# Optimization experiments

Hardware: AMD Instinct MI355X
Metric: run time of the kernel (lower is better)

## Reference

```python
import jax, jax.numpy as jnp
import numpy as np
from jax.scipy.special import digamma

# Dims (see init_kwargs): pose P=4 -> D=16, stem A=128, primary caps B=32,
# classes C=10, class-caps kernel K=6 (== primary feature map size), 3 routing iters.
P, D, A, B, C, K, ITER = 4, 16, 128, 32, 10, 6, 3
N = B * K * K                                    # input capsules routed to each class capsule
ALPHA0, KAPPA0, NU0 = 1.0, 1.0, float(D + 1)     # Dirichlet/Normal-Wishart priors (m0=0, Psi0=I, cov='diag')
BN_EPS, EPS = 1e-5, 1e-8


def conv2d(x, w, s):
    return jax.lax.conv_general_dilated(x, w, (s, s), 'VALID',
                                        dimension_numbers=('NCHW', 'OIHW', 'NCHW'))


def bn(x, gamma, beta, axes):
    # batch-norm with batch statistics (training-mode math)
    mu = x.mean(axes, keepdims=True)
    var = x.var(axes, keepdims=True)
    return (x - mu) * jax.lax.rsqrt(var + BN_EPS) * gamma + beta


def setup_inputs():
    key = jax.random.key(0)
    ks = jax.random.split(key, 4)
    f32 = jnp.float32
    x = jax.random.normal(ks[0], (128, 3, 32, 32), dtype=f32)
    conv1_w = jax.random.normal(ks[1], (A, 3, 5, 5), dtype=f32) * 0.1
    bn1_g = jnp.ones((A,), f32); bn1_b = jnp.zeros((A,), f32)
    prim_w = jax.random.normal(ks[2], (B * D + B, A, 3, 3), dtype=f32) * 0.05
    bna_g = jnp.ones((B,), f32); bna_b = jnp.zeros((B,), f32)
    bnp_g = jnp.ones((B,), f32); bnp_b = jnp.zeros((B,), f32)
    W_ij = jax.random.normal(ks[3], (B, C, K, K, P, P), dtype=f32) * 0.3
    return dict(x=x, conv1_w=conv1_w, bn1_g=bn1_g, bn1_b=bn1_b, prim_w=prim_w,
                bna_g=bna_g, bna_b=bna_b, bnp_g=bnp_g, bnp_b=bnp_b, W_ij=W_ij)


def _vb_stats(Ra, V):
    # Ra: (b,N,C) responsibility * input activation; V: (b,N,C,D) votes
    Nj = Ra.sum(1) + EPS                                         # (b,C)
    xbar = jnp.einsum('bnc,bncd->bcd', Ra, V) / Nj[..., None]    # weighted vote mean
    diff = V - xbar[:, None]
    sigma = jnp.einsum('bnc,bncd->bcd', Ra, diff * diff) / Nj[..., None]  # diag cov
    kappa = KAPPA0 + Nj
    m = Nj[..., None] * xbar / kappa[..., None]                  # posterior mean (m0 = 0)
    nu = NU0 + Nj
    Psi = 1.0 + Nj[..., None] * sigma + (KAPPA0 * Nj / kappa)[..., None] * xbar * xbar  # Psi0 = I (diag)
    return Nj, kappa, m, nu, Psi


def _expectations(Nj, nu, Psi, d_idx):
    alpha = ALPHA0 + Nj
    E_lnpi = digamma(alpha) - digamma(alpha.sum(-1, keepdims=True))
    E_lnLam = (digamma(0.5 * (nu[..., None] + 1.0 - d_idx)).sum(-1)
               + D * jnp.log(2.0) - jnp.log(Psi).sum(-1))
    return E_lnpi, E_lnLam


def reference(x, conv1_w, bn1_g, bn1_b, prim_w, bna_g, bna_b, bnp_g, bnp_b, W_ij):
    b = x.shape[0]
    # --- stem: Conv5x5/s2 + BN + ReLU ---
    h = conv2d(x, conv1_w, 2)                                    # (b,A,14,14)
    h = jax.nn.relu(bn(h, bn1_g[None, :, None, None], bn1_b[None, :, None, None], (0, 2, 3)))
    # --- primary capsules: Conv3x3/s2 -> poses + activations ---
    pc = conv2d(h, prim_w, 2)                                    # (b,B*D+B,6,6)
    poses, a = pc[:, :B * D], pc[:, B * D:]
    a = jax.nn.sigmoid(bn(a, bna_g[None, :, None, None], bna_b[None, :, None, None], (0, 2, 3)))
    poses = bn(poses.reshape(b, B, D, K, K),
               bnp_g[None, :, None, None, None], bnp_b[None, :, None, None, None], (0, 2, 3, 4))
    poses = poses.reshape(b, B, P, P, K, K)
    # --- class capsules: votes V = W_ij @ pose, kernel covers whole 6x6 map ---
    V = jnp.einsum('icxypq,biqrxy->bicxypr', W_ij, poses)        # (b,B,C,K,K,P,P)
    V = V.transpose(0, 1, 3, 4, 2, 5, 6).reshape(b, N, C, D)
    a_i = a.reshape(b, N)
    # --- variational Bayes routing (diag Normal-Wishart, ITER iterations) ---
    d_idx = jnp.arange(1, D + 1, dtype=x.dtype)
    R = jnp.full((b, N, C), 1.0 / C, dtype=x.dtype)
    for t in range(ITER):
        Nj, kappa, m, nu, Psi = _vb_stats(R * a_i[:, :, None], V)
        if t < ITER - 1:
            E_lnpi, E_lnLam = _expectations(Nj, nu, Psi, d_idx)
            dm = V - m[:, None]
            quad = D / kappa[:, None, :] + nu[:, None, :] * jnp.einsum('bncd,bcd->bnc', dm * dm, 1.0 / Psi)
            lnp = (E_lnpi[:, None] + 0.5 * E_lnLam[:, None]
                   - 0.5 * D * jnp.log(2.0 * jnp.pi) - 0.5 * quad)
            R = jax.nn.softmax(lnp, axis=-1)
    E_lnpi, E_lnLam = _expectations(Nj, nu, Psi, d_idx)
    logits = E_lnpi + 0.5 * E_lnLam                              # (b,C)
    yhat = jax.nn.sigmoid(bn(logits, 1.0, 0.0, (0,)))            # BatchNorm1d(affine=False)
    return yhat
```

## Files before the change

### kernel.cpp

```cpp
#include <hip/hip_runtime.h>
#include <hip/hip_bf16.h>

#define NB 128
#define AA 128
#define BB 32
#define CC 10
#define KK 6
#define DD 16
#define NN 1152
#define H1 14
#define CH2 544
#define NG 4608
#define KG 1152
#define MG 576

typedef short bfrag8 __attribute__((ext_vector_type(8)));
typedef float facc4 __attribute__((ext_vector_type(4)));

__device__ __forceinline__ unsigned short f2bf(float f) {
    unsigned u = __float_as_uint(f);
    u += 0x7FFF + ((u >> 16) & 1);
    return (unsigned short)(u >> 16);
}
__device__ __forceinline__ float bf2f(unsigned short s) {
    return __uint_as_float(((unsigned)s) << 16);
}

__global__ __launch_bounds__(256) void k_conv1(const float* __restrict__ x,
                                               const float* __restrict__ w,
                                               float* __restrict__ h,
                                               float* __restrict__ part1s,
                                               float* __restrict__ part1q) {
    __shared__ __align__(16) float sX[3][32][36];
    __shared__ float sW[16][76];
    __shared__ float sS[224], sQ[224];
    const int ocg = blockIdx.x;
    const int b = blockIdx.y;
    const int oc0 = ocg * 16;
    const int tid = threadIdx.x;
    for (int j = tid; j < 3072; j += 256) {
        int ic = j >> 10, rem = j & 1023;
        sX[ic][rem >> 5][rem & 31] = x[b * 3072 + j];
    }
    for (int j = tid; j < 16 * 75; j += 256) {
        sW[j / 75][j % 75] = w[oc0 * 75 + j];
    }
    __syncthreads();
    const bool act = tid < 224;
    const int oc_l = tid / 14, oy = tid % 14;
    float acc[14];
#pragma unroll
    for (int j = 0; j < 14; ++j) acc[j] = 0.f;
    if (act) {
        const float* wr = &sW[oc_l][0];
#pragma unroll
        for (int ic = 0; ic < 3; ++ic) {
#pragma unroll
            for (int ky = 0; ky < 5; ++ky) {
                const float* xr = &sX[ic][2 * oy + ky][0];
                float row[32];
#pragma unroll
                for (int q = 0; q < 8; ++q) {
                    float4 v = *reinterpret_cast<const float4*>(xr + q * 4);
                    row[q * 4 + 0] = v.x; row[q * 4 + 1] = v.y;
                    row[q * 4 + 2] = v.z; row[q * 4 + 3] = v.w;
                }
                float w0 = wr[ic * 25 + ky * 5 + 0];
                float w1 = wr[ic * 25 + ky * 5 + 1];
                float w2 = wr[ic * 25 + ky * 5 + 2];
                float w3 = wr[ic * 25 + ky * 5 + 3];
                float w4 = wr[ic * 25 + ky * 5 + 4];
#pragma unroll
                for (int ox = 0; ox < 14; ++ox) {
                    float s = acc[ox];
                    s = fmaf(row[2 * ox + 0], w0, s);
                    s = fmaf(row[2 * ox + 1], w1, s);
                    s = fmaf(row[2 * ox + 2], w2, s);
                    s = fmaf(row[2 * ox + 3], w3, s);
                    s = fmaf(row[2 * ox + 4], w4, s);
                    acc[ox] = s;
                }
            }
        }
        float* out = h + ((size_t)(b * AA + oc0 + oc_l) * 14 + oy) * 14;
#pragma unroll
        for (int q = 0; q < 7; ++q)
            *reinterpret_cast<float2*>(out + q * 2) = make_float2(acc[q * 2], acc[q * 2 + 1]);
        float s_th = 0.f, q_th = 0.f;
#pragma unroll
        for (int ox = 0; ox < 14; ++ox) { s_th += acc[ox]; q_th = fmaf(acc[ox], acc[ox], q_th); }
        sS[tid] = s_th; sQ[tid] = q_th;
    }
    __syncthreads();
    if (tid < 16) {
        float s = 0.f, q = 0.f;
#pragma unroll
        for (int r = 0; r < 14; ++r) { s += sS[tid * 14 + r]; q += sQ[tid * 14 + r]; }
        part1s[(oc0 + tid) * NB + b] = s;
        part1q[(oc0 + tid) * NB + b] = q;
    }
}

__device__ __forceinline__ void blk_reduce2(float& s, float& s2, int tid) {
#pragma unroll
    for (int o = 32; o > 0; o >>= 1) { s += __shfl_down(s, o); s2 += __shfl_down(s2, o); }
    __shared__ float ls[4], lq[4];
    int lane = tid & 63, wid = tid >> 6;
    if (lane == 0) { ls[wid] = s; lq[wid] = s2; }
    __syncthreads();
    if (tid == 0) {
        s = ls[0] + ls[1] + ls[2] + ls[3];
        s2 = lq[0] + lq[1] + lq[2] + lq[3];
    }
}

__global__ void k_bnred1(const float* __restrict__ part1s, const float* __restrict__ part1q,
                         const float* __restrict__ g, const float* __restrict__ be,
                         float* __restrict__ bn1) {
    int c = blockIdx.x;
    int tid = threadIdx.x;
    float s = (tid < NB) ? part1s[c * NB + tid] : 0.f;
    float s2 = (tid < NB) ? part1q[c * NB + tid] : 0.f;
    blk_reduce2(s, s2, tid);
    if (tid == 0) {
        const float n = (float)(NB * 196);
        float mu = s / n;
        float var = s2 / n - mu * mu;
        float sc = g[c] * rsqrtf(var + 1e-5f);
        bn1[c] = sc;
        bn1[AA + c] = be[c] - mu * sc;
    }
}

__global__ void k_pim(const float* __restrict__ w, const float* __restrict__ h,
                      const float* __restrict__ bn1,
                      unsigned short* __restrict__ Ah, unsigned short* __restrict__ Al,
                      unsigned short* __restrict__ Bh, unsigned short* __restrict__ Bl) {
    const int blk = blockIdx.x;
    const int tid = threadIdx.x;
    if (blk < 324) {
        int t = blk * 256 + tid;
        int row = t / (KG / 8), seg = t % (KG / 8);
        alignas(16) unsigned short hi[8], lo[8];
        if (row < CH2) {
            const float* src = w + (size_t)row * KG + seg * 8;
#pragma unroll
            for (int j = 0; j < 8; ++j) {
                float v = src[j];
                unsigned short hh = f2bf(v);
                hi[j] = hh;
                lo[j] = f2bf(v - bf2f(hh));
            }
        } else {
#pragma unroll
            for (int j = 0; j < 8; ++j) { hi[j] = 0; lo[j] = 0; }
        }
        *reinterpret_cast<uint4*>(Ah + (size_t)row * KG + seg * 8) = *reinterpret_cast<const uint4*>(hi);
        *reinterpret_cast<uint4*>(Al + (size_t)row * KG + seg * 8) = *reinterpret_cast<const uint4*>(lo);
        return;
    }
    __shared__ float sBn1[2 * AA];
    sBn1[tid] = bn1[tid];
    __syncthreads();
    int t = (blk - 324) * 256 + tid;
    int n = t / (KG / 8), seg = t % (KG / 8);
    int b = n / 36, xy = n % 36;
    int oy = xy / 6, ox = xy % 6;
    const float* hb = h + (size_t)b * (AA * 196) + (2 * oy) * 14 + 2 * ox;
    alignas(16) unsigned short hi[8], lo[8];
#pragma unroll
    for (int j = 0; j < 8; ++j) {
        int k = seg * 8 + j;
        int ic = k / 9, kk = k - ic * 9;
        int ky = kk / 3, kx = kk - ky * 3;
        float v = hb[ic * 196 + ky * 14 + kx];
        v = fmaxf(fmaf(v, sBn1[ic], sBn1[AA + ic]), 0.f);
        unsigned short hh = f2bf(v);
        hi[j] = hh;
        lo[j] = f2bf(v - bf2f(hh));
    }
    *reinterpret_cast<uint4*>(Bh + (size_t)n * KG + seg * 8) = *reinterpret_cast<const uint4*>(hi);
    *reinterpret_cast<uint4*>(Bl + (size_t)n * KG + seg * 8) = *reinterpret_cast<const uint4*>(lo);
}

__global__ __launch_bounds__(256, 4) void k_gemm(const unsigned short* __restrict__ Ah,
                                                 const unsigned short* __restrict__ Al,
                                                 const unsigned short* __restrict__ Bh,
                                                 const unsigned short* __restrict__ Bl,
                                                 float* __restrict__ pcT,
                                                 float* __restrict__ part2) {
    __shared__ alignas(16) unsigned short sAh[64][44], sAl[64][44];
    __shared__ alignas(16) unsigned short sBh[64][44], sBl[64][44];
    __shared__ float sRed[128];
    const int s = blockIdx.x;
    const int k8 = s & 7, j = s >> 3;
    const int jm = j / 9;
    const int y = k8 + 8 * jm;
    const int xg = j - 9 * jm;
    const int oc0 = xg * 64;
    const int n0 = y * 64;
    const int tid = threadIdx.x;
    const int lane = tid & 63, wv = tid >> 6;
    const int wm = wv >> 1, wn = wv & 1;
    const int quad = lane >> 4, r16 = lane & 15;
    const int srow = tid >> 2, sseg = tid & 3;

    facc4 acc[2][2] = {};
    const size_t gA = (size_t)(oc0 + srow) * KG + sseg * 8;
    const size_t gB = (size_t)(n0 + srow) * KG + sseg * 8;

    uint4 vAh = *reinterpret_cast<const uint4*>(Ah + gA);
    uint4 vAl = *reinterpret_cast<const uint4*>(Al + gA);
    uint4 vBh = *reinterpret_cast<const uint4*>(Bh + gB);
    uint4 vBl = *reinterpret_cast<const uint4*>(Bl + gB);

    for (int ks = 0; ks < KG / 32; ++ks) {
        __syncthreads();
        *reinterpret_cast<uint4*>(&sAh[srow][sseg * 8]) = vAh;
        *reinterpret_cast<uint4*>(&sAl[srow][sseg * 8]) = vAl;
        *reinterpret_cast<uint4*>(&sBh[srow][sseg * 8]) = vBh;
        *reinterpret_cast<uint4*>(&sBl[srow][sseg * 8]) = vBl;
        __syncthreads();
        if (ks + 1 < KG / 32) {
            const int k0n = (ks + 1) * 32;
            vAh = *reinterpret_cast<const uint4*>(Ah + gA + k0n);
            vAl = *reinterpret_cast<const uint4*>(Al + gA + k0n);
            vBh = *reinterpret_cast<const uint4*>(Bh + gB + k0n);
            vBl = *reinterpret_cast<const uint4*>(Bl + gB + k0n);
        }
        bfrag8 ah[2], al[2], bh[2], bl[2];
#pragma unroll
        for (int i = 0; i < 2; ++i) {
            ah[i] = *reinterpret_cast<const bfrag8*>(&sAh[wm * 32 + i * 16 + r16][quad * 8]);
            al[i] = *reinterpret_cast<const bfrag8*>(&sAl[wm * 32 + i * 16 + r16][quad * 8]);
            bh[i] = *reinterpret_cast<const bfrag8*>(&sBh[wn * 32 + i * 16 + r16][quad * 8]);
            bl[i] = *reinterpret_cast<const bfrag8*>(&sBl[wn * 32 + i * 16 + r16][quad * 8]);
        }
#pragma unroll
        for (int i = 0; i < 2; ++i)
#pragma unroll
            for (int jj = 0; jj < 2; ++jj) {
                acc[i][jj] = __builtin_amdgcn_mfma_f32_16x16x32_bf16(ah[i], bh[jj], acc[i][jj], 0, 0, 0);
                acc[i][jj] = __builtin_amdgcn_mfma_f32_16x16x32_bf16(ah[i], bl[jj], acc[i][jj], 0, 0, 0);
                acc[i][jj] = __builtin_amdgcn_mfma_f32_16x16x32_bf16(al[i], bh[jj], acc[i][jj], 0, 0, 0);
            }
    }
#pragma unroll
    for (int i = 0; i < 2; ++i) {
        int oc_base = oc0 + wm * 32 + i * 16 + quad * 4;
        if (oc_base >= CH2) continue;
#pragma unroll
        for (int jj = 0; jj < 2; ++jj) {
            int n = n0 + wn * 32 + jj * 16 + r16;
            *reinterpret_cast<facc4*>(pcT + (size_t)n * CH2 + oc_base) = acc[i][jj];
        }
    }
    if (xg < 8) {
        float ps[2], pq[2];
#pragma unroll
        for (int i = 0; i < 2; ++i) {
            float sv = 0.f, qv = 0.f;
#pragma unroll
            for (int jj = 0; jj < 2; ++jj)
#pragma unroll
                for (int comp = 0; comp < 4; ++comp) {
                    float v = acc[i][jj][comp];
                    sv += v; qv = fmaf(v, v, qv);
                }
#pragma unroll
            for (int o = 32; o > 0; o >>= 1) { sv += __shfl_down(sv, o); qv += __shfl_down(qv, o); }
            ps[i] = sv; pq[i] = qv;
        }
        if (lane == 0) {
#pragma unroll
            for (int i = 0; i < 2; ++i) { sRed[wv * 4 + i * 2 + 0] = ps[i]; sRed[wv * 4 + i * 2 + 1] = pq[i]; }
        }
        __syncthreads();
        if (tid < 8) {
            int wm_ = tid >> 2, i_ = (tid >> 1) & 1, sel = tid & 1;
            float v = sRed[(2 * wm_) * 4 + i_ * 2 + sel] + sRed[(2 * wm_ + 1) * 4 + i_ * 2 + sel];
            int g = xg * 4 + wm_ * 2 + i_;
            part2[sel * 2304 + g * 72 + y] = v;
        }
    } else {
        if (wm == 0) {
#pragma unroll
            for (int i = 0; i < 2; ++i)
#pragma unroll
                for (int comp = 0; comp < 4; ++comp) {
                    float v0 = acc[i][0][comp], v1 = acc[i][1][comp];
                    float sv = v0 + v1;
                    float qv = fmaf(v0, v0, v1 * v1);
#pragma unroll
                    for (int o = 8; o > 0; o >>= 1) {
                        sv += __shfl_down(sv, o, 16);
                        qv += __shfl_down(qv, o, 16);
                    }
                    if (r16 == 0) {
                        int idx = ((wv * 4 + quad) * 2 + i) * 4 + comp;
                        sRed[idx] = sv;
                        sRed[64 + idx] = qv;
                    }
                }
        }
        __syncthreads();
        if (tid < 64) {
            int ch = tid >> 1, sel = tid & 1;
            int i_ = ch >> 4, rem = ch & 15, quad_ = rem >> 2, comp_ = rem & 3;
            int base = sel * 64;
            float v = sRed[base + ((0 * 4 + quad_) * 2 + i_) * 4 + comp_] +
                      sRed[base + ((1 * 4 + quad_) * 2 + i_) * 4 + comp_];
            part2[4608 + sel * 2304 + ch * 72 + y] = v;
        }
    }
}

__global__ void k_bnred2(const float* __restrict__ part2,
                         const float* __restrict__ bna_g, const float* __restrict__ bna_b,
                         const float* __restrict__ bnp_g, const float* __restrict__ bnp_b,
                         float* __restrict__ bn2) {
    int t = threadIdx.x;
    if (t < 32) {
        float s = 0.f, s2 = 0.f;
#pragma unroll
        for (int yy = 0; yy < 72; ++yy) { s += part2[t * 72 + yy]; s2 += part2[2304 + t * 72 + yy]; }
        const float n = (float)(NB * DD * 36);
        float mu = s / n, var = s2 / n - mu * mu;
        float sc = bnp_g[t] * rsqrtf(var + 1e-5f);
        bn2[t] = sc; bn2[32 + t] = bnp_b[t] - mu * sc;
    } else {
        int ch = t - 32;
        float s = 0.f, s2 = 0.f;
#pragma unroll
        for (int yy = 0; yy < 72; ++yy) { s += part2[4608 + ch * 72 + yy]; s2 += part2[6912 + ch * 72 + yy]; }
        const float n = (float)(NB * 36);
        float mu = s / n, var = s2 / n - mu * mu;
        float sc = bna_g[ch] * rsqrtf(var + 1e-5f);
        bn2[64 + ch] = sc; bn2[96 + ch] = bna_b[ch] - mu * sc;
    }
}

__device__ __forceinline__ float digammaf_(float x) {
    float r = 0.f;
    while (x < 6.f) { r -= 1.f / x; x += 1.f; }
    float xi = 1.f / x;
    float xi2 = xi * xi;
    return r + logf(x) - 0.5f * xi -
           xi2 * (0.0833333333f - xi2 * (0.0083333333f - xi2 * 0.0039682540f));
}

template <int FIRST>
__global__ __launch_bounds__(640) void k_routed(
    const float* __restrict__ pcT, const float* __restrict__ bn2g,
    const float* __restrict__ Wij,
    const float* __restrict__ S0i, const float* __restrict__ S1i, const float* __restrict__ S2i,
    float* __restrict__ S0o, float* __restrict__ S1o, float* __restrict__ S2o) {
    const int b = blockIdx.x >> 1, half = blockIdx.x & 1;
    const int tid = threadIdx.x;
    const int c = tid >> 6, lane = tid & 63;
    __shared__ float sLnp[CC][66];
    __shared__ float sBn2[128];
    __shared__ __align__(16) float sP[64][20];
    __shared__ float sA[64];
    __shared__ float sM[CC][16], sGq[CC][16], sBase[CC];
    if (tid < 128) sBn2[tid] = bn2g[tid];
    if (!FIRST && tid < 160) {
        int cc = tid >> 4, d = tid & 15;
        int bc = b * CC + cc;
        float njraw = S0i[bc] + S0i[NB * CC + bc];
        float nj = njraw + 1e-8f;
        float kappa = 1.f + nj;
        float nu = 17.f + nj;
        float s1 = S1i[bc * 16 + d] + S1i[(NB * CC + bc) * 16 + d];
        float s2v = S2i[bc * 16 + d] + S2i[(NB * CC + bc) * 16 + d];
        float xbar = s1 / nj;
        float sig = (s2v - 2.f * xbar * s1 + xbar * xbar * njraw) / nj;
        float Psi = 1.f + nj * sig + (nj / kappa) * xbar * xbar;
        sM[cc][d] = nj * xbar / kappa;
        sGq[cc][d] = 0.5f * nu / Psi;
        float term = digammaf_(0.5f * (nu + 1.f - (float)(d + 1))) - logf(Psi);
#pragma unroll
        for (int o = 8; o > 0; o >>= 1) term += __shfl_down(term, o, 16);
        if (d == 0) {
            float asum = 0.f;
#pragma unroll
            for (int k = 0; k < CC; ++k)
                asum += 1.f + S0i[b * CC + k] + S0i[NB * CC + b * CC + k] + 1e-8f;
            float elnlam = 16.f * 0.69314718056f + term;
            float elnpi = digammaf_(1.f + nj) - digammaf_(asum);
            float lb = elnpi + 0.5f * elnlam;
            sBase[cc] = lb - 8.f * 1.83787706641f - 8.f / kappa;
        }
    }
    float mc[16], Gc[16], basec = 0.f;
    float s0 = 0.f, s1[16], s2[16];
#pragma unroll
    for (int d = 0; d < 16; ++d) { s1[d] = 0.f; s2[d] = 0.f; }

    const int nbase = half * 576;
    alignas(16) float Wc[16], Wn[16];
    {
        int n = nbase + lane;
        int i = n / 36, xy = n - i * 36;
        const float4* wp = reinterpret_cast<const float4*>(Wij + (((size_t)i * CC + c) * 36 + xy) * 16);
        *reinterpret_cast<float4*>(&Wc[0])  = wp[0];
        *reinterpret_cast<float4*>(&Wc[4])  = wp[1];
        *reinterpret_cast<float4*>(&Wc[8])  = wp[2];
        *reinterpret_cast<float4*>(&Wc[12]) = wp[3];
    }
    const int sr = tid >> 2, sq = tid & 3;
    float4 pv = {0.f, 0.f, 0.f, 0.f};
    float araw = 0.f;
    if (tid < 256) {
        int n = nbase + sr;
        int i = n / 36, xy = n - i * 36;
        pv = *reinterpret_cast<const float4*>(pcT + (size_t)(b * 36 + xy) * CH2 + i * 16 + sq * 4);
    } else if (tid < 320) {
        int n = nbase + (tid - 256);
        int i = n / 36, xy = n - i * 36;
        araw = pcT[(size_t)(b * 36 + xy) * CH2 + BB * DD + i];
    }
    __syncthreads();

#pragma unroll 1
    for (int it = 0; it < 9; ++it) {
        if (tid < 256) {
            int n = nbase + it * 64 + sr;
            int i = n / 36;
            float psc = sBn2[i], psh = sBn2[32 + i];
            float4 v = pv;
            v.x = fmaf(v.x, psc, psh); v.y = fmaf(v.y, psc, psh);
            v.z = fmaf(v.z, psc, psh); v.w = fmaf(v.w, psc, psh);
            *reinterpret_cast<float4*>(&sP[sr][sq * 4]) = v;
        } else if (tid < 320) {
            int n = nbase + it * 64 + (tid - 256);
            int i = n / 36;
            float va = fmaf(araw, sBn2[64 + i], sBn2[96 + i]);
            sA[tid - 256] = 1.f / (1.f + expf(-va));
        }
        if (!FIRST && it == 0) {
#pragma unroll
            for (int d = 0; d < 16; ++d) { mc[d] = sM[c][d]; Gc[d] = sGq[c][d]; }
            basec = sBase[c];
        }
        __syncthreads();
        alignas(16) float P[16];
        *reinterpret_cast<float4*>(&P[0])  = *reinterpret_cast<const float4*>(&sP[lane][0]);
        *reinterpret_cast<float4*>(&P[4])  = *reinterpret_cast<const float4*>(&sP[lane][4]);
        *reinterpret_cast<float4*>(&P[8])  = *reinterpret_cast<const float4*>(&sP[lane][8]);
        *reinterpret_cast<float4*>(&P[12]) = *reinterpret_cast<const float4*>(&sP[lane][12]);
        float V[16];
#pragma unroll
        for (int p = 0; p < 4; ++p)
#pragma unroll
            for (int r = 0; r < 4; ++r)
                V[p * 4 + r] = Wc[p * 4 + 0] * P[0 + r] + Wc[p * 4 + 1] * P[4 + r] +
                               Wc[p * 4 + 2] * P[8 + r] + Wc[p * 4 + 3] * P[12 + r];
        float av = sA[lane];
        if (it < 8) {
            int nx = nbase + (it + 1) * 64 + lane;
            int ix = nx / 36, xyx = nx - ix * 36;
            const float4* wp = reinterpret_cast<const float4*>(Wij + (((size_t)ix * CC + c) * 36 + xyx) * 16);
            *reinterpret_cast<float4*>(&Wn[0])  = wp[0];
            *reinterpret_cast<float4*>(&Wn[4])  = wp[1];
            *reinterpret_cast<float4*>(&Wn[8])  = wp[2];
            *reinterpret_cast<float4*>(&Wn[12]) = wp[3];
            if (tid < 256) {
                int n = nbase + (it + 1) * 64 + sr;
                int i = n / 36, xy = n - i * 36;
                pv = *reinterpret_cast<const float4*>(pcT + (size_t)(b * 36 + xy) * CH2 + i * 16 + sq * 4);
            } else if (tid < 320) {
                int n = nbase + (it + 1) * 64 + (tid - 256);
                int i = n / 36, xy = n - i * 36;
                araw = pcT[(size_t)(b * 36 + xy) * CH2 + BB * DD + i];
            }
        }
        float wgt;
        if (FIRST) {
            wgt = 0.1f * av;
            __syncthreads();
        } else {
            float q = 0.f;
#pragma unroll
            for (int d = 0; d < 16; ++d) {
                float dm = V[d] - mc[d];
                q = fmaf(dm * dm, Gc[d], q);
            }
            float lnp = basec - q;
            sLnp[c][lane] = lnp;
            __syncthreads();
            float mx = -1e30f;
#pragma unroll
            for (int cc = 0; cc < CC; ++cc) mx = fmaxf(mx, sLnp[cc][lane]);
            float ssum = 0.f;
#pragma unroll
            for (int cc = 0; cc < CC; ++cc) ssum += expf(sLnp[cc][lane] - mx);
            wgt = expf(lnp - mx) / ssum * av;
        }
        s0 += wgt;
#pragma unroll
        for (int d = 0; d < 16; ++d) {
            float wv = wgt * V[d];
            s1[d] += wv;
            s2[d] = fmaf(wv, V[d], s2[d]);
        }
        if (it < 8) {
#pragma unroll
            for (int d = 0; d < 16; ++d) Wc[d] = Wn[d];
        }
    }
#pragma unroll
    for (int o = 32; o > 0; o >>= 1) {
        s0 += __shfl_down(s0, o);
#pragma unroll
        for (int k = 0; k < 16; ++k) {
            s1[k] += __shfl_down(s1[k], o);
            s2[k] += __shfl_down(s2[k], o);
        }
    }
    if (lane == 0) {
        int idx = half * (NB * CC) + b * CC + c;
        S0o[idx] = s0;
#pragma unroll
        for (int k = 0; k < 16; ++k) { S1o[idx * 16 + k] = s1[k]; S2o[idx * 16 + k] = s2[k]; }
    }
}

__global__ void k_final2(const float* __restrict__ S0p, const float* __restrict__ S1p,
                         const float* __restrict__ S2p, float* __restrict__ out) {
    int c = blockIdx.x;
    int b = threadIdx.x;
    int bc = b * CC + c;
    float njraw = S0p[bc] + S0p[NB * CC + bc];
    float nj = njraw + 1e-8f;
    float asum = 0.f;
#pragma unroll
    for (int k = 0; k < CC; ++k)
        asum += 1.f + S0p[b * CC + k] + S0p[NB * CC + b * CC + k] + 1e-8f;
    float kappa = 1.f + nj;
    float nu = 17.f + nj;
    float elnlam = 16.f * 0.69314718056f;
    for (int d = 0; d < 16; ++d) {
        float s1 = S1p[bc * 16 + d] + S1p[(NB * CC + bc) * 16 + d];
        float s2v = S2p[bc * 16 + d] + S2p[(NB * CC + bc) * 16 + d];
        float xbar = s1 / nj;
        float sig = (s2v - 2.f * xbar * s1 + xbar * xbar * njraw) / nj;
        float Psi = 1.f + nj * sig + (nj / kappa) * xbar * xbar;
        elnlam += digammaf_(0.5f * (nu + 1.f - (float)(d + 1))) - logf(Psi);
    }
    float elnpi = digammaf_(1.f + nj) - digammaf_(asum);
    float v = elnpi + 0.5f * elnlam;
    float s = v, s2 = v * v;
#pragma unroll
    for (int o = 32; o > 0; o >>= 1) { s += __shfl_down(s, o); s2 += __shfl_down(s2, o); }
    __shared__ float ls[2], lq[2];
    int lane = b & 63, wid = b >> 6;
    if (lane == 0) { ls[wid] = s; lq[wid] = s2; }
    __syncthreads();
    float mu = (ls[0] + ls[1]) * (1.f / 128.f);
    float var = (lq[0] + lq[1]) * (1.f / 128.f) - mu * mu;
    out[b * CC + c] = 1.f / (1.f + expf(-(v - mu) * rsqrtf(var + 1e-5f)));
}

extern "C" void kernel_launch(void* const* d_in, const int* in_sizes, int n_in,
                              void* d_out, int out_size, void* d_ws, size_t ws_size,
                              hipStream_t stream) {
    (void)in_sizes; (void)n_in; (void)out_size; (void)ws_size;
    const float* x       = (const float*)d_in[0];
    const float* conv1_w = (const float*)d_in[1];
    const float* bn1_g   = (const float*)d_in[2];
    const float* bn1_b   = (const float*)d_in[3];
    const float* prim_w  = (const float*)d_in[4];
    const float* bna_g   = (const float*)d_in[5];
    const float* bna_b   = (const float*)d_in[6];
    const float* bnp_g   = (const float*)d_in[7];
    const float* bnp_b   = (const float*)d_in[8];
    const float* Wij     = (const float*)d_in[9];

    float* ws = (float*)d_ws;
    float* h   = ws;
    float* pcT = ws + 3211264;
    unsigned short* Bh = (unsigned short*)(ws + 5718016);
    unsigned short* Bl = (unsigned short*)(ws + 8372224);
    unsigned short* Ahp = (unsigned short*)(ws + 11026432);
    unsigned short* Alp = (unsigned short*)(ws + 11358208);
    float* bn1    = ws + 11689984;
    float* bn2    = ws + 11690240;
    float* S0a    = ws + 11690368;
    float* S1a    = ws + 11692928;
    float* S2a    = ws + 11733888;
    float* S0b    = ws + 11774848;
    float* S1b    = ws + 11777408;
    float* S2b    = ws + 11818368;
    float* part1s = ws + 11859328;
    float* part1q = ws + 11875712;
    float* part2  = ws + 11892096;
    float* out    = (float*)d_out;

    k_conv1<<<dim3(8, 128), 256, 0, stream>>>(x, conv1_w, h, part1s, part1q);
    k_bnred1<<<128, 256, 0, stream>>>(part1s, part1q, bn1_g, bn1_b, bn1);
    k_pim<<<2916, 256, 0, stream>>>(prim_w, h, bn1, Ahp, Alp, Bh, Bl);
    k_gemm<<<648, 256, 0, stream>>>(Ahp, Alp, Bh, Bl, pcT, part2);
    k_bnred2<<<1, 64, 0, stream>>>(part2, bna_g, bna_b, bnp_g, bnp_b, bn2);

    k_routed<1><<<256, 640, 0, stream>>>(pcT, bn2, Wij, S0a, S1a, S2a, S0a, S1a, S2a);
    k_routed<0><<<256, 640, 0, stream>>>(pcT, bn2, Wij, S0a, S1a, S2a, S0b, S1b, S2b);
    k_routed<0><<<256, 640, 0, stream>>>(pcT, bn2, Wij, S0b, S1b, S2b, S0a, S1a, S2a);
    k_final2<<<10, 128, 0, stream>>>(S0a, S1a, S2a, out);
}
```

Before: 179.9 us.

## Load poses per thread directly and double-buffer lnp to drop per-iteration barriers

Each of the 10 class waves now loads its own 16-float pose row and activation from global memory into registers, prefetching the next one. This replaces the cooperative shared-memory staging of poses and activations, together with its barrier. The softmax scratch is double-buffered by iteration parity, so only one barrier per iteration remains in the routed kernel and none in the FIRST variant. The cost is ten times more redundant global (cache-served) pose loads, repeated BN and sigmoid work per wave, and higher register pressure.

```diff
diff --git a/kernel.cpp b/kernel.cpp
--- a/kernel.cpp
+++ b/kernel.cpp
@@ -358,10 +358,8 @@
     const int b = blockIdx.x >> 1, half = blockIdx.x & 1;
     const int tid = threadIdx.x;
     const int c = tid >> 6, lane = tid & 63;
-    __shared__ float sLnp[CC][66];
+    __shared__ float sLnp[2][CC][66];
     __shared__ float sBn2[128];
-    __shared__ __align__(16) float sP[64][20];
-    __shared__ float sA[64];
     __shared__ float sM[CC][16], sGq[CC][16], sBase[CC];
     if (tid < 128) sBn2[tid] = bn2g[tid];
     if (!FIRST && tid < 160) {
@@ -392,13 +390,13 @@
             sBase[cc] = lb - 8.f * 1.83787706641f - 8.f / kappa;
         }
     }
-    float mc[16], Gc[16], basec = 0.f;
     float s0 = 0.f, s1[16], s2[16];
 #pragma unroll
     for (int d = 0; d < 16; ++d) { s1[d] = 0.f; s2[d] = 0.f; }
 
     const int nbase = half * 576;
-    alignas(16) float Wc[16], Wn[16];
+    alignas(16) float Wc[16], Wn[16], Praw[16], Prawn[16];
+    float araw, arawn = 0.f;
     {
         int n = nbase + lane;
         int i = n / 36, xy = n - i * 36;
@@ -407,48 +405,31 @@
         *reinterpret_cast<float4*>(&Wc[4])  = wp[1];
         *reinterpret_cast<float4*>(&Wc[8])  = wp[2];
         *reinterpret_cast<float4*>(&Wc[12]) = wp[3];
-    }
-    const int sr = tid >> 2, sq = tid & 3;
-    float4 pv = {0.f, 0.f, 0.f, 0.f};
-    float araw = 0.f;
-    if (tid < 256) {
-        int n = nbase + sr;
-        int i = n / 36, xy = n - i * 36;
-        pv = *reinterpret_cast<const float4*>(pcT + (size_t)(b * 36 + xy) * CH2 + i * 16 + sq * 4);
-    } else if (tid < 320) {
-        int n = nbase + (tid - 256);
-        int i = n / 36, xy = n - i * 36;
-        araw = pcT[(size_t)(b * 36 + xy) * CH2 + BB * DD + i];
+        const float* pr = pcT + (size_t)(b * 36 + xy) * CH2;
+        *reinterpret_cast<float4*>(&Praw[0])  = *reinterpret_cast<const float4*>(pr + i * 16 + 0);
+        *reinterpret_cast<float4*>(&Praw[4])  = *reinterpret_cast<const float4*>(pr + i * 16 + 4);
+        *reinterpret_cast<float4*>(&Praw[8])  = *reinterpret_cast<const float4*>(pr + i * 16 + 8);
+        *reinterpret_cast<float4*>(&Praw[12]) = *reinterpret_cast<const float4*>(pr + i * 16 + 12);
+        araw = pr[BB * DD + i];
     }
     __syncthreads();
+    float mc[16], Gc[16], basec = 0.f;
+    if (!FIRST) {
+#pragma unroll
+        for (int d = 0; d < 16; ++d) { mc[d] = sM[c][d]; Gc[d] = sGq[c][d]; }
+        basec = sBase[c];
+    }
 
 #pragma unroll 1
     for (int it = 0; it < 9; ++it) {
-        if (tid < 256) {
-            int n = nbase + it * 64 + sr;
-            int i = n / 36;
-            float psc = sBn2[i], psh = sBn2[32 + i];
-            float4 v = pv;
-            v.x = fmaf(v.x, psc, psh); v.y = fmaf(v.y, psc, psh);
-            v.z = fmaf(v.z, psc, psh); v.w = fmaf(v.w, psc, psh);
-            *reinterpret_cast<float4*>(&sP[sr][sq * 4]) = v;
-        } else if (tid < 320) {
-            int n = nbase + it * 64 + (tid - 256);
-            int i = n / 36;
-            float va = fmaf(araw, sBn2[64 + i], sBn2[96 + i]);
-            sA[tid - 256] = 1.f / (1.f + expf(-va));
-        }
-        if (!FIRST && it == 0) {
-#pragma unroll
-            for (int d = 0; d < 16; ++d) { mc[d] = sM[c][d]; Gc[d] = sGq[c][d]; }
-            basec = sBase[c];
-        }
-        __syncthreads();
-        alignas(16) float P[16];
-        *reinterpret_cast<float4*>(&P[0])  = *reinterpret_cast<const float4*>(&sP[lane][0]);
-        *reinterpret_cast<float4*>(&P[4])  = *reinterpret_cast<const float4*>(&sP[lane][4]);
-        *reinterpret_cast<float4*>(&P[8])  = *reinterpret_cast<const float4*>(&sP[lane][8]);
-        *reinterpret_cast<float4*>(&P[12]) = *reinterpret_cast<const float4*>(&sP[lane][12]);
+        const int n = nbase + it * 64 + lane;
+        const int i = n / 36;
+        const float psc = sBn2[i], psh = sBn2[32 + i];
+        float P[16];
+#pragma unroll
+        for (int d = 0; d < 16; ++d) P[d] = fmaf(Praw[d], psc, psh);
+        float va = fmaf(araw, sBn2[64 + i], sBn2[96 + i]);
+        float av = 1.f / (1.f + expf(-va));
         float V[16];
 #pragma unroll
         for (int p = 0; p < 4; ++p)
@@ -456,7 +437,6 @@
             for (int r = 0; r < 4; ++r)
                 V[p * 4 + r] = Wc[p * 4 + 0] * P[0 + r] + Wc[p * 4 + 1] * P[4 + r] +
                                Wc[p * 4 + 2] * P[8 + r] + Wc[p * 4 + 3] * P[12 + r];
-        float av = sA[lane];
         if (it < 8) {
             int nx = nbase + (it + 1) * 64 + lane;
             int ix = nx / 36, xyx = nx - ix * 36;
@@ -465,20 +445,16 @@
             *reinterpret_cast<float4*>(&Wn[4])  = wp[1];
             *reinterpret_cast<float4*>(&Wn[8])  = wp[2];
             *reinterpret_cast<float4*>(&Wn[12]) = wp[3];
-            if (tid < 256) {
-                int n = nbase + (it + 1) * 64 + sr;
-                int i = n / 36, xy = n - i * 36;
-                pv = *reinterpret_cast<const float4*>(pcT + (size_t)(b * 36 + xy) * CH2 + i * 16 + sq * 4);
-            } else if (tid < 320) {
-                int n = nbase + (it + 1) * 64 + (tid - 256);
-                int i = n / 36, xy = n - i * 36;
-                araw = pcT[(size_t)(b * 36 + xy) * CH2 + BB * DD + i];
-            }
+            const float* pr = pcT + (size_t)(b * 36 + xyx) * CH2;
+            *reinterpret_cast<float4*>(&Prawn[0])  = *reinterpret_cast<const float4*>(pr + ix * 16 + 0);
+            *reinterpret_cast<float4*>(&Prawn[4])  = *reinterpret_cast<const float4*>(pr + ix * 16 + 4);
+            *reinterpret_cast<float4*>(&Prawn[8])  = *reinterpret_cast<const float4*>(pr + ix * 16 + 8);
+            *reinterpret_cast<float4*>(&Prawn[12]) = *reinterpret_cast<const float4*>(pr + ix * 16 + 12);
+            arawn = pr[BB * DD + ix];
         }
         float wgt;
         if (FIRST) {
             wgt = 0.1f * av;
-            __syncthreads();
         } else {
             float q = 0.f;
 #pragma unroll
@@ -487,14 +463,14 @@
                 q = fmaf(dm * dm, Gc[d], q);
             }
             float lnp = basec - q;
-            sLnp[c][lane] = lnp;
+            sLnp[it & 1][c][lane] = lnp;
             __syncthreads();
             float mx = -1e30f;
 #pragma unroll
-            for (int cc = 0; cc < CC; ++cc) mx = fmaxf(mx, sLnp[cc][lane]);
+            for (int cc = 0; cc < CC; ++cc) mx = fmaxf(mx, sLnp[it & 1][cc][lane]);
             float ssum = 0.f;
 #pragma unroll
-            for (int cc = 0; cc < CC; ++cc) ssum += expf(sLnp[cc][lane] - mx);
+            for (int cc = 0; cc < CC; ++cc) ssum += expf(sLnp[it & 1][cc][lane] - mx);
             wgt = expf(lnp - mx) / ssum * av;
         }
         s0 += wgt;
@@ -506,7 +482,8 @@
         }
         if (it < 8) {
 #pragma unroll
-            for (int d = 0; d < 16; ++d) Wc[d] = Wn[d];
+            for (int d = 0; d < 16; ++d) { Wc[d] = Wn[d]; Praw[d] = Prawn[d]; }
+            araw = arawn;
         }
     }
 #pragma unroll
```

New measurement: 201.4 us. 12.0% more time.

## Fuse routing iterations and final reduction into one cooperative kernel with grid syncs

Applied to the files above, without the earlier changes.

Merges the three routing launches and the final logits/batch-norm kernel into a single cooperative kernel that uses grid.sync between iterations. The aim is to remove three kernel launch gaps and their tail effects. In exchange it adds grid-wide barriers and thread fences, carries cooperative-launch overhead, and the final stage runs on only 10 blocks while the rest sit idle. It also moves the per-class mean and precision register loads out of the loop.

```diff
diff --git a/kernel.cpp b/kernel.cpp
--- a/kernel.cpp
+++ b/kernel.cpp
@@ -1,5 +1,8 @@
 #include <hip/hip_runtime.h>
 #include <hip/hip_bf16.h>
+#include <hip/hip_cooperative_groups.h>
+
+namespace cg = cooperative_groups;
 
 #define NB 128
 #define AA 128
@@ -350,20 +353,14 @@
 }
 
 template <int FIRST>
-__global__ __launch_bounds__(640) void k_routed(
-    const float* __restrict__ pcT, const float* __restrict__ bn2g,
-    const float* __restrict__ Wij,
+__device__ __forceinline__ void routed_body(
+    const float* __restrict__ pcT, const float* __restrict__ Wij,
     const float* __restrict__ S0i, const float* __restrict__ S1i, const float* __restrict__ S2i,
-    float* __restrict__ S0o, float* __restrict__ S1o, float* __restrict__ S2o) {
-    const int b = blockIdx.x >> 1, half = blockIdx.x & 1;
-    const int tid = threadIdx.x;
+    float* __restrict__ S0o, float* __restrict__ S1o, float* __restrict__ S2o,
+    int b, int half, int tid,
+    float (*sLnp)[66], const float* sBn2, float (*sP)[20], float* sA,
+    float (*sM)[16], float (*sGq)[16], float* sBase) {
     const int c = tid >> 6, lane = tid & 63;
-    __shared__ float sLnp[CC][66];
-    __shared__ float sBn2[128];
-    __shared__ __align__(16) float sP[64][20];
-    __shared__ float sA[64];
-    __shared__ float sM[CC][16], sGq[CC][16], sBase[CC];
-    if (tid < 128) sBn2[tid] = bn2g[tid];
     if (!FIRST && tid < 160) {
         int cc = tid >> 4, d = tid & 15;
         int bc = b * CC + cc;
@@ -392,7 +389,6 @@
             sBase[cc] = lb - 8.f * 1.83787706641f - 8.f / kappa;
         }
     }
-    float mc[16], Gc[16], basec = 0.f;
     float s0 = 0.f, s1[16], s2[16];
 #pragma unroll
     for (int d = 0; d < 16; ++d) { s1[d] = 0.f; s2[d] = 0.f; }
@@ -421,6 +417,12 @@
         araw = pcT[(size_t)(b * 36 + xy) * CH2 + BB * DD + i];
     }
     __syncthreads();
+    float mc[16], Gc[16], basec = 0.f;
+    if (!FIRST) {
+#pragma unroll
+        for (int d = 0; d < 16; ++d) { mc[d] = sM[c][d]; Gc[d] = sGq[c][d]; }
+        basec = sBase[c];
+    }
 
 #pragma unroll 1
     for (int it = 0; it < 9; ++it) {
@@ -437,11 +439,6 @@
             int i = n / 36;
             float va = fmaf(araw, sBn2[64 + i], sBn2[96 + i]);
             sA[tid - 256] = 1.f / (1.f + expf(-va));
-        }
-        if (!FIRST && it == 0) {
-#pragma unroll
-            for (int d = 0; d < 16; ++d) { mc[d] = sM[c][d]; Gc[d] = sGq[c][d]; }
-            basec = sBase[c];
         }
         __syncthreads();
         alignas(16) float P[16];
@@ -526,40 +523,70 @@
     }
 }
 
-__global__ void k_final2(const float* __restrict__ S0p, const float* __restrict__ S1p,
-                         const float* __restrict__ S2p, float* __restrict__ out) {
-    int c = blockIdx.x;
-    int b = threadIdx.x;
-    int bc = b * CC + c;
-    float njraw = S0p[bc] + S0p[NB * CC + bc];
-    float nj = njraw + 1e-8f;
-    float asum = 0.f;
-#pragma unroll
-    for (int k = 0; k < CC; ++k)
-        asum += 1.f + S0p[b * CC + k] + S0p[NB * CC + b * CC + k] + 1e-8f;
-    float kappa = 1.f + nj;
-    float nu = 17.f + nj;
-    float elnlam = 16.f * 0.69314718056f;
-    for (int d = 0; d < 16; ++d) {
-        float s1 = S1p[bc * 16 + d] + S1p[(NB * CC + bc) * 16 + d];
-        float s2v = S2p[bc * 16 + d] + S2p[(NB * CC + bc) * 16 + d];
-        float xbar = s1 / nj;
-        float sig = (s2v - 2.f * xbar * s1 + xbar * xbar * njraw) / nj;
-        float Psi = 1.f + nj * sig + (nj / kappa) * xbar * xbar;
-        elnlam += digammaf_(0.5f * (nu + 1.f - (float)(d + 1))) - logf(Psi);
-    }
-    float elnpi = digammaf_(1.f + nj) - digammaf_(asum);
-    float v = elnpi + 0.5f * elnlam;
+__global__ __launch_bounds__(640) void k_routed_all(
+    const float* __restrict__ pcT, const float* __restrict__ bn2g,
+    const float* __restrict__ Wij,
+    float* __restrict__ S0a, float* __restrict__ S1a, float* __restrict__ S2a,
+    float* __restrict__ S0b, float* __restrict__ S1b, float* __restrict__ S2b,
+    float* __restrict__ out) {
+    cg::grid_group grid = cg::this_grid();
+    __shared__ float sLnp[CC][66];
+    __shared__ float sBn2[128];
+    __shared__ __align__(16) float sP[64][20];
+    __shared__ float sA[64];
+    __shared__ float sM[CC][16], sGq[CC][16], sBase[CC];
+    __shared__ float fls[2], flq[2];
+    const int b = blockIdx.x >> 1, half = blockIdx.x & 1;
+    const int tid = threadIdx.x;
+    if (tid < 128) sBn2[tid] = bn2g[tid];
+    routed_body<1>(pcT, Wij, S0a, S1a, S2a, S0a, S1a, S2a, b, half, tid,
+                   sLnp, sBn2, sP, sA, sM, sGq, sBase);
+    __threadfence();
+    grid.sync();
+    routed_body<0>(pcT, Wij, S0a, S1a, S2a, S0b, S1b, S2b, b, half, tid,
+                   sLnp, sBn2, sP, sA, sM, sGq, sBase);
+    __threadfence();
+    grid.sync();
+    routed_body<0>(pcT, Wij, S0b, S1b, S2b, S0a, S1a, S2a, b, half, tid,
+                   sLnp, sBn2, sP, sA, sM, sGq, sBase);
+    __threadfence();
+    grid.sync();
+    if (blockIdx.x >= 10) return;
+    const int c = blockIdx.x;
+    float v = 0.f;
+    if (tid < 128) {
+        int bb = tid;
+        int bc = bb * CC + c;
+        float njraw = S0a[bc] + S0a[NB * CC + bc];
+        float nj = njraw + 1e-8f;
+        float asum = 0.f;
+#pragma unroll
+        for (int k = 0; k < CC; ++k)
+            asum += 1.f + S0a[bb * CC + k] + S0a[NB * CC + bb * CC + k] + 1e-8f;
+        float kappa = 1.f + nj;
+        float nu = 17.f + nj;
+        float elnlam = 16.f * 0.69314718056f;
+        for (int d = 0; d < 16; ++d) {
+            float s1 = S1a[bc * 16 + d] + S1a[(NB * CC + bc) * 16 + d];
+            float s2v = S2a[bc * 16 + d] + S2a[(NB * CC + bc) * 16 + d];
+            float xbar = s1 / nj;
+            float sig = (s2v - 2.f * xbar * s1 + xbar * xbar * njraw) / nj;
+            float Psi = 1.f + nj * sig + (nj / kappa) * xbar * xbar;
+            elnlam += digammaf_(0.5f * (nu + 1.f - (float)(d + 1))) - logf(Psi);
+        }
+        float elnpi = digammaf_(1.f + nj) - digammaf_(asum);
+        v = elnpi + 0.5f * elnlam;
+    }
     float s = v, s2 = v * v;
 #pragma unroll
     for (int o = 32; o > 0; o >>= 1) { s += __shfl_down(s, o); s2 += __shfl_down(s2, o); }
-    __shared__ float ls[2], lq[2];
-    int lane = b & 63, wid = b >> 6;
-    if (lane == 0) { ls[wid] = s; lq[wid] = s2; }
+    if (tid < 128 && (tid & 63) == 0) { fls[tid >> 6] = s; flq[tid >> 6] = s2; }
     __syncthreads();
-    float mu = (ls[0] + ls[1]) * (1.f / 128.f);
-    float var = (lq[0] + lq[1]) * (1.f / 128.f) - mu * mu;
-    out[b * CC + c] = 1.f / (1.f + expf(-(v - mu) * rsqrtf(var + 1e-5f)));
+    if (tid < 128) {
+        float mu = (fls[0] + fls[1]) * (1.f / 128.f);
+        float var = (flq[0] + flq[1]) * (1.f / 128.f) - mu * mu;
+        out[tid * CC + c] = 1.f / (1.f + expf(-(v - mu) * rsqrtf(var + 1e-5f)));
+    }
 }
 
 extern "C" void kernel_launch(void* const* d_in, const int* in_sizes, int n_in,
@@ -603,8 +630,12 @@
     k_gemm<<<648, 256, 0, stream>>>(Ahp, Alp, Bh, Bl, pcT, part2);
     k_bnred2<<<1, 64, 0, stream>>>(part2, bna_g, bna_b, bnp_g, bnp_b, bn2);
 
-    k_routed<1><<<256, 640, 0, stream>>>(pcT, bn2, Wij, S0a, S1a, S2a, S0a, S1a, S2a);
-    k_routed<0><<<256, 640, 0, stream>>>(pcT, bn2, Wij, S0a, S1a, S2a, S0b, S1b, S2b);
-    k_routed<0><<<256, 640, 0, stream>>>(pcT, bn2, Wij, S0b, S1b, S2b, S0a, S1a, S2a);
-    k_final2<<<10, 128, 0, stream>>>(S0a, S1a, S2a, out);
-}
+    const float* pcT_c = pcT;
+    const float* bn2_c = bn2;
+    const float* Wij_c = Wij;
+    void* args[] = {(void*)&pcT_c, (void*)&bn2_c, (void*)&Wij_c,
+                    (void*)&S0a, (void*)&S1a, (void*)&S2a,
+                    (void*)&S0b, (void*)&S1b, (void*)&S2b, (void*)&out};
+    hipLaunchCooperativeKernel(reinterpret_cast<void*>(k_routed_all),
+                               dim3(256), dim3(640), args, 0, stream);
+}
```

New measurement: 415.1 us. 131% more time.
